# Performance work log

Hardware: AMD Instinct MI355X
Metric: run time of the kernel (lower is better)

Reference implementation:

```python
import jax, jax.numpy as jnp
import numpy as np

D = 256  # hardcoded Dense units in the original layer

def setup_inputs() -> dict:
    key = jax.random.key(0)
    ks = jax.random.split(key, 7)
    B, S, F = 8, 2048, 256
    x = jax.random.normal(ks[0], (B, S, F), dtype=jnp.float32)
    # Dense layers (kernel + bias), glorot-ish scale
    scale = 1.0 / np.sqrt(F)
    Wq = jax.random.normal(ks[1], (F, D), dtype=jnp.float32) * scale
    Wk = jax.random.normal(ks[2], (F, D), dtype=jnp.float32) * scale
    Wv = jax.random.normal(ks[3], (F, D), dtype=jnp.float32) * scale
    bq = jax.random.normal(ks[4], (D,), dtype=jnp.float32) * 0.01
    bk = jax.random.normal(ks[5], (D,), dtype=jnp.float32) * 0.01
    bv = jax.random.normal(ks[6], (D,), dtype=jnp.float32) * 0.01
    return {"x": x, "Wq": Wq, "bq": bq, "Wk": Wk, "bk": bk, "Wv": Wv, "bv": bv}

def reference(x, Wq, bq, Wk, bk, Wv, bv):
    # Q/K/V projections: Dense(256) == x @ W + b
    Q = jnp.einsum('bsf,fd->bsd', x, Wq) + bq
    K = jnp.einsum('bsf,fd->bsd', x, Wk) + bk
    V = jnp.einsum('bsf,fd->bsd', x, Wv) + bv
    scores = jnp.einsum('bqd,bkd->bqk', Q, K) / jnp.sqrt(jnp.float32(D))
    attn = jax.nn.softmax(scores, axis=-1)
    return jnp.einsum('bqk,bkd->bqd', attn, V)
```

## Files before the change

kernel.cpp:

```cpp
#include <hip/hip_runtime.h>

typedef __bf16 bf16;
typedef __bf16 bf16x4v __attribute__((ext_vector_type(4)));
typedef __bf16 bf16x8 __attribute__((ext_vector_type(8)));
typedef float f32x4 __attribute__((ext_vector_type(4)));
typedef short s16x4 __attribute__((ext_vector_type(4)));

#define MFMA_X32(A, B, C) __builtin_amdgcn_mfma_f32_16x16x32_bf16(A, B, C, 0, 0, 0)

static __device__ __forceinline__ float fast_exp2(float x) {
  float r;
  asm volatile("v_exp_f32 %0, %1\n\ts_nop 0" : "=v"(r) : "v"(x));
  return r;
}

static __device__ __forceinline__ void gll16(const void* g, void* l) {
  __builtin_amdgcn_global_load_lds(
      (const __attribute__((address_space(1))) void*)g,
      (__attribute__((address_space(3))) void*)l, 16, 0, 0);
}

#define WT_OFF 0
#define Q_OFF 393216
#define K_OFF 8781824
#define V_OFF 17170432

__global__ __launch_bounds__(256) void prep_wt(const float* __restrict__ Wq,
                                               const float* __restrict__ Wk,
                                               const float* __restrict__ Wv,
                                               bf16* __restrict__ Wt) {
  const int idx = blockIdx.x * 256 + threadIdx.x;
  const int p = idx >> 16;
  const int rem = idx & 65535;
  const int k = rem >> 8, n = rem & 255;
  const float* W = (p == 0) ? Wq : ((p == 1) ? Wk : Wv);
  Wt[p * 65536 + n * 256 + k] = (bf16)W[rem];
}

__global__ __launch_bounds__(256, 3) void proj_qkv(const float* __restrict__ x,
                                                   const float* __restrict__ bq,
                                                   const float* __restrict__ bk,
                                                   const float* __restrict__ bv,
                                                   char* __restrict__ ws0) {
  __shared__ __align__(16) char smem[40960];
  const bf16* Wt = (const bf16*)(ws0 + WT_OFF);
  bf16* Qo = (bf16*)(ws0 + Q_OFF);
  bf16* Ko = (bf16*)(ws0 + K_OFF);
  bf16* Vc = (bf16*)(ws0 + V_OFF);
  const int t = threadIdx.x;
  const int lane = t & 63, w = t >> 6, l16 = lane & 15, quad = lane >> 4;
  const int fam = blockIdx.x % 6;
  const int rgroup = blockIdx.x / 6;
  const int p = fam >> 1, ch = fam & 1;
  const float* bias = (p == 0) ? bq : ((p == 1) ? bk : bv);
  const float sc = (p == 0) ? 0.09016844005556021f : 1.0f;

  const int nl = w * 32 + l16;
  bf16x8 bfr[2][8];
#pragma unroll
  for (int nt = 0; nt < 2; ++nt)
#pragma unroll
    for (int kt = 0; kt < 8; ++kt)
      bfr[nt][kt] = *(const bf16x8*)&Wt[p * 65536 + (ch * 128 + nl + nt * 16) * 256 +
                                        kt * 32 + quad * 8];
  float bias2[2];
#pragma unroll
  for (int nt = 0; nt < 2; ++nt) bias2[nt] = bias[ch * 128 + nl + nt * 16];

  const int row0 = rgroup * 128;
  char* outL = smem + 32768;

  float4 xr[4][2];
#define STAGE_LOAD(tile)                                                        \
  {                                                                             \
    const float* xp = x + (row0 + (tile) * 32) * 256;                           \
    _Pragma("unroll") for (int i = 0; i < 4; ++i) {                             \
      const int u2 = i * 256 + t, row = u2 >> 5, col8 = (u2 & 31) * 8;          \
      xr[i][0] = *(const float4*)&xp[row * 256 + col8];                         \
      xr[i][1] = *(const float4*)&xp[row * 256 + col8 + 4];                     \
    }                                                                           \
  }
#define STAGE_WRITE(buf)                                                        \
  {                                                                             \
    _Pragma("unroll") for (int i = 0; i < 4; ++i) {                             \
      const int u2 = i * 256 + t, row = u2 >> 5, col8 = (u2 & 31) * 8;          \
      const float* f0 = (const float*)&xr[i][0];                                \
      const float* f1 = (const float*)&xr[i][1];                                \
      bf16x8 h;                                                                 \
      _Pragma("unroll") for (int j = 0; j < 4; ++j) {                           \
        h[j] = (bf16)f0[j];                                                     \
        h[4 + j] = (bf16)f1[j];                                                 \
      }                                                                         \
      *(bf16x8*)&smem[(buf) * 16384 + row * 512 +                               \
                      ((col8 * 2) ^ ((row & 7) << 4))] = h;                     \
    }                                                                           \
  }

  STAGE_LOAD(0);
  STAGE_WRITE(0);
  __syncthreads();

  int cur = 0;
  for (int tt = 0; tt < 4; ++tt) {
    if (tt < 3) STAGE_LOAD(tt + 1);

    f32x4 acc[2][2];
#pragma unroll
    for (int rs = 0; rs < 2; ++rs)
#pragma unroll
      for (int nt = 0; nt < 2; ++nt) acc[rs][nt] = f32x4{0.f, 0.f, 0.f, 0.f};
    const char* xb = smem + cur * 16384;
#pragma unroll
    for (int rs = 0; rs < 2; ++rs) {
      const int row = rs * 16 + l16;
#pragma unroll
      for (int kt = 0; kt < 8; ++kt) {
        const bf16x8 a = *(const bf16x8*)(xb + row * 512 +
                                          ((kt * 64 + quad * 16) ^ ((l16 & 7) << 4)));
        acc[rs][0] = MFMA_X32(a, bfr[0][kt], acc[rs][0]);
        acc[rs][1] = MFMA_X32(a, bfr[1][kt], acc[rs][1]);
      }
    }
    __syncthreads();

#pragma unroll
    for (int rs = 0; rs < 2; ++rs)
#pragma unroll
      for (int nt = 0; nt < 2; ++nt)
#pragma unroll
        for (int r = 0; r < 4; ++r) {
          const int sl = rs * 16 + quad * 4 + r;
          const int nn = nl + nt * 16;
          const bf16 hv = (bf16)((acc[rs][nt][r] + bias2[nt]) * sc);
          int pos;
          if (p == 0)
            pos = sl * 128 + nn;
          else if (p == 1)
            pos = (sl >> 4) * 2048 + (nn >> 5) * 512 + ((nn >> 3) & 3) * 128 +
                  (sl & 15) * 8 + (nn & 7);
          else
            pos = (nn >> 4) * 512 + ((sl >> 2) & 3) * 128 + (nn & 15) * 8 +
                  (sl >> 4) * 4 + (sl & 3);
          *(bf16*)(outL + pos * 2) = hv;
        }
    if (tt < 3) STAGE_WRITE(cur ^ 1);
    __syncthreads();

    const int rowg = row0 + tt * 32;
    if (p == 0) {
      const int row = t >> 3, cb = (t & 7) * 32;
      const float4 v0 = *(const float4*)(outL + row * 256 + cb);
      const float4 v1 = *(const float4*)(outL + row * 256 + cb + 16);
      char* dst = (char*)Qo + (rowg + row) * 512 + ch * 256 + cb;
      *(float4*)dst = v0;
      *(float4*)(dst + 16) = v1;
    } else if (p == 1) {
      const int b2 = rowg >> 11, s0 = rowg & 2047;
      char* dst = (char*)Ko + b2 * 1048576 + ((s0 >> 4) + (t >> 7)) * 8192 +
                  ch * 4096 + (t & 127) * 32;
      const float4 v0 = *(const float4*)(outL + t * 32);
      const float4 v1 = *(const float4*)(outL + t * 32 + 16);
      *(float4*)dst = v0;
      *(float4*)(dst + 16) = v1;
    } else {
      const int b2 = rowg >> 11, s0 = rowg & 2047;
      char* dst = (char*)Vc + b2 * 1048576 + (s0 >> 5) * 16384 + ch * 8192 + t * 32;
      const float4 v0 = *(const float4*)(outL + t * 32);
      const float4 v1 = *(const float4*)(outL + t * 32 + 16);
      *(float4*)dst = v0;
      *(float4*)(dst + 16) = v1;
    }
    cur ^= 1;
  }
#undef STAGE_LOAD
#undef STAGE_WRITE
}

#define SLOT_SZ 16640

__global__ __launch_bounds__(512, 2) void flash_attn(const char* __restrict__ ws0,
                                                     float* __restrict__ out) {
  __shared__ __align__(1024) char smem[163840];
  const bf16* Qp = (const bf16*)(ws0 + Q_OFF);
  const int t = threadIdx.x;
  const int lane = t & 63, w = t >> 6;
  const int l16 = lane & 15, quad = lane >> 4;
  const int qs = w & 1, kq = w >> 1;
  const int b = blockIdx.x & 7;
  const int qt = blockIdx.x >> 3;
  const int qrow0 = b * 2048 + qt * 64 + qs * 32;

  bf16x8 qf[2][8];
#pragma unroll
  for (int qsub = 0; qsub < 2; ++qsub)
#pragma unroll
    for (int kt = 0; kt < 8; ++kt)
      qf[qsub][kt] =
          *(const bf16x8*)&Qp[(qrow0 + qsub * 16 + l16) * 256 + kt * 32 + quad * 8];

  f32x4 o[2][16];
#pragma unroll
  for (int qsub = 0; qsub < 2; ++qsub)
#pragma unroll
    for (int dt = 0; dt < 16; ++dt) o[qsub][dt] = f32x4{0.f, 0.f, 0.f, 0.f};
  float m_[2] = {-1e30f, -1e30f}, l_[2] = {0.f, 0.f};

  unsigned goffK[4], loffK[4];
#pragma unroll
  for (int i = 0; i < 4; ++i) {
    const int u = w * 4 + i;
    const int kq2 = u >> 3, e = u & 7;
    goffK[i] = (unsigned)K_OFF + b * 1048576u + kq2 * 262144u + e * 1024u + lane * 16u;
    loffK[i] = kq2 * 8192u + e * 1024u;
  }
  unsigned goffV[4], loffV[4];
#pragma unroll
  for (int i = 0; i < 4; ++i) {
    const int u = w * 4 + i;
    const int kqv = u >> 3, e = u & 7;
    goffV[i] = (unsigned)V_OFF + b * 1048576u + kqv * 262144u + e * 1024u + lane * 16u;
    loffV[i] = kqv * 8192u + e * 1024u;
  }

#define STAGE_K(S)                                                             \
  {                                                                            \
    _Pragma("unroll") for (int i = 0; i < 4; ++i)                              \
        gll16(ws0 + goffK[i] + (unsigned)(S) * 8192u,                          \
              smem + (unsigned)(((S) & 1) * 32768) + loffK[i]);                \
  }
#define STAGE_V_H0(P)                                                          \
  {                                                                            \
    _Pragma("unroll") for (int i = 0; i < 4; ++i)                              \
        gll16(ws0 + goffV[i] + (unsigned)(P) * 16384u,                         \
              smem + 65536u + (unsigned)(((P) & 1) * 32768) + loffV[i]);       \
  }
#define STAGE_V_H1(P)                                                          \
  {                                                                            \
    _Pragma("unroll") for (int i = 0; i < 4; ++i)                              \
        gll16(ws0 + goffV[i] + (unsigned)(P) * 16384u + 8192u,                 \
              smem + 131072u + loffV[i]);                                      \
  }
#define QK_STEP(CURK, KC)                                                      \
  {                                                                            \
    const char* kb = smem + (CURK) + kq * 8192 + lane * 16;                    \
    f32x4 a0 = f32x4{0.f, 0.f, 0.f, 0.f}, a1 = a0;                             \
    __builtin_amdgcn_s_setprio(1);                                             \
    _Pragma("unroll") for (int kt = 0; kt < 4; ++kt) {                         \
      const bf16x8 kf = *(const bf16x8*)(kb + kt * 1024);                      \
      a0 = MFMA_X32(kf, qf[0][kt], a0);                                        \
      a1 = MFMA_X32(kf, qf[1][kt], a1);                                        \
    }                                                                          \
    _Pragma("unroll") for (int kt = 4; kt < 8; ++kt) {                         \
      const bf16x8 kf = *(const bf16x8*)(kb + kt * 1024);                      \
      sfr[0][KC] = MFMA_X32(kf, qf[0][kt], sfr[0][KC]);                        \
      sfr[1][KC] = MFMA_X32(kf, qf[1][kt], sfr[1][KC]);                        \
    }                                                                          \
    __builtin_amdgcn_s_setprio(0);                                             \
    sfr[0][KC] += a0;                                                          \
    sfr[1][KC] += a1;                                                          \
  }

  STAGE_K(0);
  STAGE_V_H0(0);

  for (int p = 0; p < 16; ++p) {
    f32x4 sfr[2][2];
#pragma unroll
    for (int qsub = 0; qsub < 2; ++qsub)
#pragma unroll
      for (int kc = 0; kc < 2; ++kc) sfr[qsub][kc] = f32x4{0.f, 0.f, 0.f, 0.f};

    __syncthreads();
    STAGE_K(2 * p + 1);
    STAGE_V_H1(p);
    QK_STEP((unsigned)((2 * p) & 1) * 32768u, 0);

    __syncthreads();
    if (p < 15) {
      STAGE_K(2 * p + 2);
      STAGE_V_H0(p + 1);
    }
    QK_STEP((unsigned)((2 * p + 1) & 1) * 32768u, 1);

    bf16x8 pa[2];
#pragma unroll
    for (int qsub = 0; qsub < 2; ++qsub) {
      const f32x4 sA = sfr[qsub][0], sB = sfr[qsub][1];
      const float cml = fmaxf(fmaxf(fmaxf(sA[0], sA[1]), fmaxf(sA[2], sA[3])),
                              fmaxf(fmaxf(sB[0], sB[1]), fmaxf(sB[2], sB[3])));
      const float mold = m_[qsub];
      if (__builtin_expect(__any(cml > mold + 6.0f), 0)) {
        float cm = fmaxf(cml, __shfl_xor(cml, 16));
        cm = fmaxf(cm, __shfl_xor(cm, 32));
        const float Mnew = fmaxf(mold, cm);
        const float al = fast_exp2(mold - Mnew);
        m_[qsub] = Mnew;
        l_[qsub] *= al;
        float ar[4];
#pragma unroll
        for (int r = 0; r < 4; ++r)
          ar[r] = __shfl(al, (quad << 4) + (quad << 2) + r);
#pragma unroll
        for (int dt = 0; dt < 16; ++dt)
#pragma unroll
          for (int r = 0; r < 4; ++r) o[qsub][dt][r] *= ar[r];
      }
      const float Mref = m_[qsub];
      float ps = 0.f;
#pragma unroll
      for (int r = 0; r < 4; ++r) {
        const bf16 p0 = (bf16)fast_exp2(sA[r] - Mref);
        const bf16 p1 = (bf16)fast_exp2(sB[r] - Mref);
        pa[qsub][r] = p0;
        pa[qsub][4 + r] = p1;
        ps += (float)p0 + (float)p1;
      }
      l_[qsub] += ps;
    }

    const char* vb0 = smem + 65536u + (unsigned)((p & 1) * 32768) + kq * 8192 +
                      lane * 16;
    const char* vb1 = smem + 131072u + kq * 8192 + lane * 16;
    __builtin_amdgcn_s_setprio(1);
#pragma unroll
    for (int dt = 0; dt < 8; ++dt) {
      const bf16x8 vf = *(const bf16x8*)(vb0 + dt * 1024);
      o[0][dt] = MFMA_X32(pa[0], vf, o[0][dt]);
      o[1][dt] = MFMA_X32(pa[1], vf, o[1][dt]);
    }
#pragma unroll
    for (int dt = 8; dt < 16; ++dt) {
      const bf16x8 vf = *(const bf16x8*)(vb1 + (dt - 8) * 1024);
      o[0][dt] = MFMA_X32(pa[0], vf, o[0][dt]);
      o[1][dt] = MFMA_X32(pa[1], vf, o[1][dt]);
    }
    __builtin_amdgcn_s_setprio(0);
  }
#undef STAGE_K
#undef STAGE_V_H0
#undef STAGE_V_H1
#undef QK_STEP

#pragma unroll
  for (int qsub = 0; qsub < 2; ++qsub) {
    l_[qsub] += __shfl_xor(l_[qsub], 16);
    l_[qsub] += __shfl_xor(l_[qsub], 32);
  }

  __syncthreads();

  float* mlf = (float*)(smem + 133120);
  if (quad == 0) {
#pragma unroll
    for (int qsub = 0; qsub < 2; ++qsub) {
      const int base = ((kq * 2 + qs) * 2 + qsub) * 32;
      mlf[base + l16] = m_[qsub];
      mlf[base + 16 + l16] = l_[qsub];
    }
  }
  __syncthreads();
#pragma unroll
  for (int qsub = 0; qsub < 2; ++qsub) {
    float M = -1e30f, mk[4], lk[4];
#pragma unroll
    for (int k2 = 0; k2 < 4; ++k2) {
      const int base = ((k2 * 2 + qs) * 2 + qsub) * 32;
      mk[k2] = mlf[base + l16];
      lk[k2] = mlf[base + 16 + l16];
      M = fmaxf(M, mk[k2]);
    }
    float L = 0.f;
#pragma unroll
    for (int k2 = 0; k2 < 4; ++k2) L += lk[k2] * fast_exp2(mk[k2] - M);
    const float sg = fast_exp2(m_[qsub] - M) / L;
    float sr[4];
#pragma unroll
    for (int r = 0; r < 4; ++r) sr[r] = __shfl(sg, (quad << 4) + (quad << 2) + r);
#pragma unroll
    for (int dt = 0; dt < 16; ++dt)
#pragma unroll
      for (int r = 0; r < 4; ++r) o[qsub][dt][r] *= sr[r];
  }
  if (kq >= 2) {
#pragma unroll
    for (int qsub = 0; qsub < 2; ++qsub) {
      float* sb = (float*)(smem + ((kq - 2) * 4 + qs * 2 + qsub) * SLOT_SZ);
#pragma unroll
      for (int dt = 0; dt < 16; ++dt)
#pragma unroll
        for (int r = 0; r < 4; ++r)
          sb[(quad * 4 + r) * 260 + dt * 16 + l16] = o[qsub][dt][r];
    }
  }
  __syncthreads();
  if (kq < 2) {
#pragma unroll
    for (int qsub = 0; qsub < 2; ++qsub) {
      const float* sb = (const float*)(smem + (kq * 4 + qs * 2 + qsub) * SLOT_SZ);
#pragma unroll
      for (int dt = 0; dt < 16; ++dt)
#pragma unroll
        for (int r = 0; r < 4; ++r)
          o[qsub][dt][r] += sb[(quad * 4 + r) * 260 + dt * 16 + l16];
    }
  }
  __syncthreads();
  if (kq == 1) {
#pragma unroll
    for (int qsub = 0; qsub < 2; ++qsub) {
      float* sb = (float*)(smem + (qs * 2 + qsub) * SLOT_SZ);
#pragma unroll
      for (int dt = 0; dt < 16; ++dt)
#pragma unroll
        for (int r = 0; r < 4; ++r)
          sb[(quad * 4 + r) * 260 + dt * 16 + l16] = o[qsub][dt][r];
    }
  }
  __syncthreads();
  if (kq == 0) {
#pragma unroll
    for (int qsub = 0; qsub < 2; ++qsub) {
      const float* sb = (const float*)(smem + (qs * 2 + qsub) * SLOT_SZ);
#pragma unroll
      for (int dt = 0; dt < 16; ++dt)
#pragma unroll
        for (int r = 0; r < 4; ++r) {
          const float v = o[qsub][dt][r] + sb[(quad * 4 + r) * 260 + dt * 16 + l16];
          out[(qrow0 + qsub * 16 + quad * 4 + r) * 256 + dt * 16 + l16] = v;
        }
    }
  }
}

extern "C" void kernel_launch(void* const* d_in, const int* in_sizes, int n_in,
                              void* d_out, int out_size, void* d_ws,
                              size_t ws_size, hipStream_t stream) {
  const float* x = (const float*)d_in[0];
  const float* Wq = (const float*)d_in[1];
  const float* bq = (const float*)d_in[2];
  const float* Wk = (const float*)d_in[3];
  const float* bk = (const float*)d_in[4];
  const float* Wv = (const float*)d_in[5];
  const float* bv = (const float*)d_in[6];
  float* out = (float*)d_out;
  char* ws = (char*)d_ws;

  prep_wt<<<768, 256, 0, stream>>>(Wq, Wk, Wv, (bf16*)(ws + WT_OFF));
  proj_qkv<<<768, 256, 0, stream>>>(x, bq, bk, bv, ws);
  flash_attn<<<256, 512, 0, stream>>>(ws, out);
}
```

Baseline: 160.3 us.

## Fuse weight transpose into projection kernel and simplify QK accumulation chain

```diff
diff --git a/kernel.cpp b/kernel.cpp
--- a/kernel.cpp
+++ b/kernel.cpp
@@ -20,30 +20,19 @@
       (__attribute__((address_space(3))) void*)l, 16, 0, 0);
 }
 
-#define WT_OFF 0
 #define Q_OFF 393216
 #define K_OFF 8781824
 #define V_OFF 17170432
 
-__global__ __launch_bounds__(256) void prep_wt(const float* __restrict__ Wq,
-                                               const float* __restrict__ Wk,
-                                               const float* __restrict__ Wv,
-                                               bf16* __restrict__ Wt) {
-  const int idx = blockIdx.x * 256 + threadIdx.x;
-  const int p = idx >> 16;
-  const int rem = idx & 65535;
-  const int k = rem >> 8, n = rem & 255;
-  const float* W = (p == 0) ? Wq : ((p == 1) ? Wk : Wv);
-  Wt[p * 65536 + n * 256 + k] = (bf16)W[rem];
-}
-
 __global__ __launch_bounds__(256, 3) void proj_qkv(const float* __restrict__ x,
+                                                   const float* __restrict__ Wq,
+                                                   const float* __restrict__ Wk,
+                                                   const float* __restrict__ Wv,
                                                    const float* __restrict__ bq,
                                                    const float* __restrict__ bk,
                                                    const float* __restrict__ bv,
                                                    char* __restrict__ ws0) {
   __shared__ __align__(16) char smem[40960];
-  const bf16* Wt = (const bf16*)(ws0 + WT_OFF);
   bf16* Qo = (bf16*)(ws0 + Q_OFF);
   bf16* Ko = (bf16*)(ws0 + K_OFF);
   bf16* Vc = (bf16*)(ws0 + V_OFF);
@@ -52,23 +41,13 @@
   const int fam = blockIdx.x % 6;
   const int rgroup = blockIdx.x / 6;
   const int p = fam >> 1, ch = fam & 1;
+  const float* W = (p == 0) ? Wq : ((p == 1) ? Wk : Wv);
   const float* bias = (p == 0) ? bq : ((p == 1) ? bk : bv);
   const float sc = (p == 0) ? 0.09016844005556021f : 1.0f;
 
-  const int nl = w * 32 + l16;
-  bf16x8 bfr[2][8];
-#pragma unroll
-  for (int nt = 0; nt < 2; ++nt)
-#pragma unroll
-    for (int kt = 0; kt < 8; ++kt)
-      bfr[nt][kt] = *(const bf16x8*)&Wt[p * 65536 + (ch * 128 + nl + nt * 16) * 256 +
-                                        kt * 32 + quad * 8];
-  float bias2[2];
-#pragma unroll
-  for (int nt = 0; nt < 2; ++nt) bias2[nt] = bias[ch * 128 + nl + nt * 16];
-
   const int row0 = rgroup * 128;
   char* outL = smem + 32768;
+  const int nl = w * 32 + l16;
 
   float4 xr[4][2];
 #define STAGE_LOAD(tile)                                                        \
@@ -97,6 +76,22 @@
   }
 
   STAGE_LOAD(0);
+
+  bf16x8 bfr[2][8];
+#pragma unroll
+  for (int nt = 0; nt < 2; ++nt)
+#pragma unroll
+    for (int kt = 0; kt < 8; ++kt) {
+      bf16x8 h;
+#pragma unroll
+      for (int j = 0; j < 8; ++j)
+        h[j] = (bf16)W[(kt * 32 + quad * 8 + j) * 256 + ch * 128 + nl + nt * 16];
+      bfr[nt][kt] = h;
+    }
+  float bias2[2];
+#pragma unroll
+  for (int nt = 0; nt < 2; ++nt) bias2[nt] = bias[ch * 128 + nl + nt * 16];
+
   STAGE_WRITE(0);
   __syncthreads();
 
@@ -243,21 +238,13 @@
 #define QK_STEP(CURK, KC)                                                      \
   {                                                                            \
     const char* kb = smem + (CURK) + kq * 8192 + lane * 16;                    \
-    f32x4 a0 = f32x4{0.f, 0.f, 0.f, 0.f}, a1 = a0;                             \
     __builtin_amdgcn_s_setprio(1);                                             \
-    _Pragma("unroll") for (int kt = 0; kt < 4; ++kt) {                         \
-      const bf16x8 kf = *(const bf16x8*)(kb + kt * 1024);                      \
-      a0 = MFMA_X32(kf, qf[0][kt], a0);                                        \
-      a1 = MFMA_X32(kf, qf[1][kt], a1);                                        \
-    }                                                                          \
-    _Pragma("unroll") for (int kt = 4; kt < 8; ++kt) {                         \
+    _Pragma("unroll") for (int kt = 0; kt < 8; ++kt) {                         \
       const bf16x8 kf = *(const bf16x8*)(kb + kt * 1024);                      \
       sfr[0][KC] = MFMA_X32(kf, qf[0][kt], sfr[0][KC]);                        \
       sfr[1][KC] = MFMA_X32(kf, qf[1][kt], sfr[1][KC]);                        \
     }                                                                          \
     __builtin_amdgcn_s_setprio(0);                                             \
-    sfr[0][KC] += a0;                                                          \
-    sfr[1][KC] += a1;                                                          \
   }
 
   STAGE_K(0);
@@ -445,7 +432,6 @@
   float* out = (float*)d_out;
   char* ws = (char*)d_ws;
 
-  prep_wt<<<768, 256, 0, stream>>>(Wq, Wk, Wv, (bf16*)(ws + WT_OFF));
-  proj_qkv<<<768, 256, 0, stream>>>(x, bq, bk, bv, ws);
+  proj_qkv<<<768, 256, 0, stream>>>(x, Wq, Wk, Wv, bq, bk, bv, ws);
   flash_attn<<<256, 512, 0, stream>>>(ws, out);
 }
```

Result: slower. 166.4 us (+3.8%).
